# Kernel optimization log

Measured on AMD Instinct MI355X. Metric: run time of the kernel, lower is better.

## Reference

```python
import jax, jax.numpy as jnp
import numpy as np

L, B, T, D, H, FF = 4, 8, 1024, 256, 8, 1024
DK = D // H
SCALE = 1.0 / np.sqrt(DK)


def _ln(x, g, b, eps=1e-6):
    m = jnp.mean(x, axis=-1, keepdims=True)
    v = jnp.mean(jnp.square(x - m), axis=-1, keepdims=True)
    return (x - m) * jax.lax.rsqrt(v + eps) * g + b


def _l2norm(x, eps=1e-8):
    n = jnp.sqrt(jnp.sum(jnp.square(x), axis=-1, keepdims=True))
    return x / jnp.maximum(n, eps)


def setup_inputs() -> dict:
    key = jax.random.key(0)
    ks = jax.random.split(key, 8)
    s = 0.02
    inp = {
        'x': jax.random.normal(ks[0], (B, T, D), dtype=jnp.float32),
        'padding_mask': jnp.zeros((B, T), dtype=bool),
        'ln1_g': jnp.ones((L, D), jnp.float32), 'ln1_b': jnp.zeros((L, D), jnp.float32),
        'qn_g': jnp.ones((L, D), jnp.float32), 'qn_b': jnp.zeros((L, D), jnp.float32),
        'Wqkv': jax.random.normal(ks[1], (L, 3 * D, D), jnp.float32) * s,
        'bqkv': jnp.zeros((L, 3 * D), jnp.float32),
        'Wo': jax.random.normal(ks[2], (L, D, D), jnp.float32) * s,
        'bo': jnp.zeros((L, D), jnp.float32),
        'ln2_g': jnp.ones((L, D), jnp.float32), 'ln2_b': jnp.zeros((L, D), jnp.float32),
        'W1': jax.random.normal(ks[3], (L, FF, D), jnp.float32) * s,
        'b1': jnp.zeros((L, FF), jnp.float32),
        'W2': jax.random.normal(ks[4], (L, D, FF), jnp.float32) * s,
        'b2': jnp.zeros((L, D), jnp.float32),
        'alpha': jnp.full((L,), 0.1, jnp.float32),
        'beta': jnp.full((L,), 0.1, jnp.float32),
    }
    return inp


def _block(x, pad_mask, p):
    (g1, bb1, qg, qb, wqkv, bqkv, wo, bo, g2, bb2, w1, b1, w2, b2, a, be) = p
    Bn, Tn, Dn = x.shape
    # --- SemiCausalAttention on norm1(x) ---
    xn = _ln(x, g1, bb1)
    h = _ln(xn, qg, qb)                      # q_norm LayerNorm
    qkv = h @ wqkv.T + bqkv                  # [B,T,3D]
    qkv = qkv.reshape(Bn, Tn, 3, H, DK).transpose(2, 0, 3, 1, 4)  # [3,B,H,T,dk]
    Q, K, V = qkv[0], qkv[1], qkv[2]
    Q = _l2norm(Q)
    K = _l2norm(K)
    scores = jnp.einsum('bhtd,bhsd->bhts', Q, K) * SCALE
    scores = jnp.clip(scores, -10.0, 10.0)
    causal = jnp.triu(jnp.ones((Tn, Tn), dtype=bool), k=1)        # True = future
    scores = jnp.where(causal[None, None], -10000.0, scores)
    scores = jnp.where(pad_mask[:, None, None, :], -10000.0, scores)
    attn = jax.nn.softmax(scores, axis=-1)
    ao = jnp.einsum('bhts,bhsd->bhtd', attn, V)                   # [B,H,T,dk]
    ao = ao.transpose(0, 2, 1, 3).reshape(Bn, Tn, Dn)
    attn_out = (ao @ wo.T + bo) * 0.5
    x = x + jnp.tanh(a) * attn_out
    # --- FFN ---
    f = _ln(x, g2, bb2)
    f = jax.nn.gelu(f @ w1.T + b1, approximate=False)
    f = f @ w2.T + b2
    x = x + jnp.tanh(be) * f
    return jnp.clip(x, -100.0, 100.0)


def reference(x, padding_mask, ln1_g, ln1_b, qn_g, qn_b, Wqkv, bqkv, Wo, bo,
              ln2_g, ln2_b, W1, b1, W2, b2, alpha, beta):
    params = (ln1_g, ln1_b, qn_g, qn_b, Wqkv, bqkv, Wo, bo,
              ln2_g, ln2_b, W1, b1, W2, b2, alpha, beta)

    def step(carry, p):
        return _block(carry, padding_mask, p), None

    out, _ = jax.lax.scan(step, x, params)
    return out
```

## Files before the change

### kernel.cpp

```cpp
#include <hip/hip_runtime.h>
#include <hip/hip_bf16.h>
#include <math.h>

#define BB 8
#define TT 1024
#define DD 256
#define HH 8
#define BT 8192

typedef __attribute__((ext_vector_type(4))) float f32x4;
typedef __attribute__((ext_vector_type(16))) float f32x16;
typedef __attribute__((ext_vector_type(8))) short short8;
typedef __attribute__((ext_vector_type(4))) short short4v;
typedef __attribute__((ext_vector_type(8))) __bf16 bf16x8;

__device__ inline float bf2f(short s) {
  unsigned int u = ((unsigned int)(unsigned short)s) << 16;
  return __builtin_bit_cast(float, u);
}
__device__ inline short f2bf(float f) {
  unsigned int u = __builtin_bit_cast(unsigned int, f);
  unsigned int lsb = (u >> 16) & 1u;
  u += 0x7fffu + lsb;
  return (short)(u >> 16);
}
__device__ inline unsigned int cvtpk(float lo, float hi) {
  unsigned int r;
  asm("v_cvt_pk_bf16_f32 %0, %1, %2" : "=v"(r) : "v"(lo), "v"(hi));
  return r;
}

__device__ inline f32x4 mfma16(short8 a, short8 b, f32x4 c) {
  return __builtin_amdgcn_mfma_f32_16x16x32_bf16(
      __builtin_bit_cast(bf16x8, a), __builtin_bit_cast(bf16x8, b), c, 0, 0, 0);
}
__device__ inline f32x16 mfma32(short8 a, short8 b, f32x16 c) {
  return __builtin_amdgcn_mfma_f32_32x32x16_bf16(
      __builtin_bit_cast(bf16x8, a), __builtin_bit_cast(bf16x8, b), c, 0, 0, 0);
}

__device__ inline void gload_lds16(void* lds, const void* g) {
  __builtin_amdgcn_global_load_lds(
      (const __attribute__((address_space(1))) unsigned int*)g,
      (__attribute__((address_space(3))) unsigned int*)lds, 16, 0, 0);
}

__global__ __launch_bounds__(256) void cvt_all(
    const float4* __restrict__ s0, short4v* __restrict__ d0, int n0,
    const float4* __restrict__ s1, short4v* __restrict__ d1, int n1,
    const float4* __restrict__ s2, short4v* __restrict__ d2, int n2,
    const float4* __restrict__ s3, short4v* __restrict__ d3, int n3)
{
  int i = blockIdx.x * 256 + threadIdx.x;
  const float4* s; short4v* d;
  if (i < n0) { s = s0 + i; d = d0 + i; }
  else if ((i -= n0) < n1) { s = s1 + i; d = d1 + i; }
  else if ((i -= n1) < n2) { s = s2 + i; d = d2 + i; }
  else if ((i -= n2) < n3) { s = s3 + i; d = d3 + i; }
  else return;
  float4 v = *s;
  short4v o;
  o[0] = f2bf(v.x); o[1] = f2bf(v.y); o[2] = f2bf(v.z); o[3] = f2bf(v.w);
  *d = o;
}

__global__ __launch_bounds__(256) void ln_kernel(
    const float* __restrict__ Xin,
    const float* __restrict__ g1, const float* __restrict__ b1,
    const float* __restrict__ g2, const float* __restrict__ b2,
    short* __restrict__ out)
{
  const int row = blockIdx.x * 4 + (threadIdx.x >> 6);
  const int lane = threadIdx.x & 63;
  const float4 v = *(const float4*)(Xin + (size_t)row * 256 + lane * 4);
  float y[4] = {v.x, v.y, v.z, v.w};

  float s = y[0] + y[1] + y[2] + y[3];
  #pragma unroll
  for (int m = 32; m >= 1; m >>= 1) s += __shfl_xor(s, m, 64);
  float mean = s * (1.0f / 256.0f);
  float sq = 0.f;
  #pragma unroll
  for (int i = 0; i < 4; ++i) { y[i] -= mean; sq += y[i] * y[i]; }
  #pragma unroll
  for (int m = 32; m >= 1; m >>= 1) sq += __shfl_xor(sq, m, 64);
  float rs = rsqrtf(sq * (1.0f / 256.0f) + 1e-6f);
  #pragma unroll
  for (int i = 0; i < 4; ++i) y[i] = y[i] * rs * g1[lane * 4 + i] + b1[lane * 4 + i];

  float s2 = y[0] + y[1] + y[2] + y[3];
  #pragma unroll
  for (int m = 32; m >= 1; m >>= 1) s2 += __shfl_xor(s2, m, 64);
  float m2 = s2 * (1.0f / 256.0f);
  float sq2 = 0.f;
  #pragma unroll
  for (int i = 0; i < 4; ++i) { y[i] -= m2; sq2 += y[i] * y[i]; }
  #pragma unroll
  for (int m = 32; m >= 1; m >>= 1) sq2 += __shfl_xor(sq2, m, 64);
  float rs2 = rsqrtf(sq2 * (1.0f / 256.0f) + 1e-6f);
  #pragma unroll
  for (int i = 0; i < 4; ++i) y[i] = y[i] * rs2 * g2[lane * 4 + i] + b2[lane * 4 + i];

  #pragma unroll
  for (int i = 0; i < 4; ++i) out[(size_t)row * 256 + lane * 4 + i] = f2bf(y[i]);
}

__global__ __launch_bounds__(256) void vtr_kernel(
    const short* __restrict__ Vc, short* __restrict__ vT)
{
  __shared__ short T_s[32][264];
  const int tid = threadIdx.x;
  const int bh = blockIdx.x >> 2;
  const int tc = blockIdx.x & 3;
  const int t = tc * 256 + tid;
  const short* src = Vc + ((size_t)(bh << 10) + t) * 32;
  short8 v0 = *(const short8*)(src);
  short8 v1 = *(const short8*)(src + 8);
  short8 v2 = *(const short8*)(src + 16);
  short8 v3 = *(const short8*)(src + 24);
  #pragma unroll
  for (int d = 0; d < 8; ++d) {
    T_s[d][tid] = v0[d];
    T_s[d + 8][tid] = v1[d];
    T_s[d + 16][tid] = v2[d];
    T_s[d + 24][tid] = v3[d];
  }
  __syncthreads();
  const int d = tid >> 3, toff = (tid & 7) * 32;
  short* dst = vT + ((size_t)bh * 32 + d) * 1024 + tc * 256 + toff;
  #pragma unroll
  for (int s = 0; s < 4; ++s)
    *(short8*)(dst + s * 8) = *(const short8*)&T_s[d][toff + s * 8];
}

template<int BN, int EPI>
__global__ __launch_bounds__(256) void gemm_bt(
    const short* __restrict__ A, const short* __restrict__ Bw,
    const float* __restrict__ bias,
    short* __restrict__ O0, short* __restrict__ O1, short* __restrict__ O2,
    int M, int N, int K)
{
  constexpr int MI = (BN == 128) ? 4 : 2;
  __shared__ __align__(16) short A_s[2][128 * 64];
  __shared__ __align__(16) short B_s[2][BN * 64];
  const int tid = threadIdx.x;
  const int lane = tid & 63;
  const int w = tid >> 6;
  const int lo4 = lane & 15, hi2 = lane >> 4;
  int wm, wn0;
  if (BN == 128) { wm = (w >> 1) * 64; wn0 = (w & 1) * 64; }
  else           { wm = w * 32;        wn0 = 0; }
  const int bid = blockIdx.x + blockIdx.y * gridDim.x;
  const int nwg = gridDim.x * gridDim.y;
  const int wg = (bid & 7) * (nwg >> 3) + (bid >> 3);
  const int tM = (wg / gridDim.x) * 128, tN = (wg % gridDim.x) * BN;

  f32x4 acc[MI][4];
  #pragma unroll
  for (int i = 0; i < MI; ++i)
    #pragma unroll
    for (int j = 0; j < 4; ++j) acc[i][j] = (f32x4){0.f, 0.f, 0.f, 0.f};

  auto stage = [&](int buf, int k0) {
    #pragma unroll
    for (int ri = 0; ri < 4; ++ri) {
      int o = ri * 2048 + tid * 8;
      int row = o >> 6;
      int col = (o & 63) ^ ((row & 7) << 3);
      gload_lds16(&A_s[buf][ri * 2048 + w * 512], A + (size_t)(tM + row) * K + k0 + col);
    }
    #pragma unroll
    for (int ri = 0; ri < BN / 32; ++ri) {
      int o = ri * 2048 + tid * 8;
      int row = o >> 6;
      int col = (o & 63) ^ ((row & 7) << 3);
      gload_lds16(&B_s[buf][ri * 2048 + w * 512], Bw + (size_t)(tN + row) * K + k0 + col);
    }
  };

  const int nt = K >> 6;
  stage(0, 0);
  __syncthreads();
  for (int t = 0; t < nt; ++t) {
    const int cur = t & 1;
    if (t + 1 < nt) stage(cur ^ 1, (t + 1) << 6);
    #pragma unroll
    for (int kc = 0; kc < 2; ++kc) {
      short8 af[MI], bfr[4];
      #pragma unroll
      for (int i = 0; i < MI; ++i) {
        int row = wm + i * 16 + lo4;
        af[i] = *(const short8*)&A_s[cur][row * 64 + ((kc * 32 + hi2 * 8) ^ ((row & 7) << 3))];
      }
      #pragma unroll
      for (int j = 0; j < 4; ++j) {
        int row = wn0 + j * 16 + lo4;
        bfr[j] = *(const short8*)&B_s[cur][row * 64 + ((kc * 32 + hi2 * 8) ^ ((row & 7) << 3))];
      }
      #pragma unroll
      for (int i = 0; i < MI; ++i)
        #pragma unroll
        for (int j = 0; j < 4; ++j)
          acc[i][j] = mfma16(af[i], bfr[j], acc[i][j]);
    }
    __syncthreads();
  }

  if (EPI == 4) {
    #pragma unroll
    for (int i = 0; i < MI; ++i)
      #pragma unroll
      for (int j = 0; j < 4; ++j)
        #pragma unroll
        for (int r = 0; r < 4; ++r)
          acc[i][j][r] += bias[tN + wn0 + j * 16 + lo4];
    if (tN < 512) {
      const float C2 = 0.25503489702966368f;
      const float sc = (tN < 256) ? C2 : 1.0f;
      #pragma unroll
      for (int i = 0; i < MI; ++i) {
        #pragma unroll
        for (int r = 0; r < 4; ++r) {
          float s01 = acc[i][0][r] * acc[i][0][r] + acc[i][1][r] * acc[i][1][r];
          float s23 = acc[i][2][r] * acc[i][2][r] + acc[i][3][r] * acc[i][3][r];
          #pragma unroll
          for (int m = 1; m <= 8; m <<= 1) {
            s01 += __shfl_xor(s01, m, 64);
            s23 += __shfl_xor(s23, m, 64);
          }
          float n01 = sc / fmaxf(sqrtf(s01), 1e-8f);
          float n23 = sc / fmaxf(sqrtf(s23), 1e-8f);
          acc[i][0][r] *= n01; acc[i][1][r] *= n01;
          acc[i][2][r] *= n23; acc[i][3][r] *= n23;
        }
      }
    }
    short* dst = (tN < 256) ? O0 : (tN < 512) ? O1 : O2;
    #pragma unroll
    for (int i = 0; i < MI; ++i)
      #pragma unroll
      for (int j = 0; j < 4; ++j)
        #pragma unroll
        for (int r = 0; r < 4; ++r) {
          int row = tM + wm + i * 16 + hi2 * 4 + r;
          int colr = (tN + wn0 + j * 16 + lo4) & 255;
          int h = colr >> 5, d = colr & 31;
          size_t idx = (((size_t)((row >> 10) * 8 + h) << 10) | (size_t)(row & 1023)) * 32 + d;
          dst[idx] = f2bf(acc[i][j][r]);
        }
    return;
  }

  #pragma unroll
  for (int i = 0; i < MI; ++i) {
    #pragma unroll
    for (int j = 0; j < 4; ++j) {
      #pragma unroll
      for (int r = 0; r < 4; ++r) {
        int row = tM + wm + i * 16 + hi2 * 4 + r;
        int col = tN + wn0 + j * 16 + lo4;
        float v = acc[i][j][r] + bias[col];
        size_t idx = (size_t)row * N + col;
        if (EPI == 2) {
          float gl = 0.5f * v * (1.0f + erff(v * 0.70710678118f));
          O0[idx] = f2bf(gl);
        } else {
          O0[idx] = f2bf(v);
        }
      }
    }
  }
}

template<int MODE>
__global__ __launch_bounds__(256) void gemm_ln(
    const short* __restrict__ A, const short* __restrict__ Bw,
    const float* __restrict__ bias, float* __restrict__ X,
    short* __restrict__ Obf, const float* __restrict__ scale_p,
    const float* __restrict__ gA, const float* __restrict__ bA,
    const float* __restrict__ gB, const float* __restrict__ bB,
    int K, int doLN)
{
  __shared__ __align__(16) short A_s[2][32 * 64];
  __shared__ __align__(16) short B_s[2][256 * 64];
  __shared__ float Red[2][32][4][2];
  const int tid = threadIdx.x;
  const int lane = tid & 63;
  const int w = tid >> 6;
  const int lo4 = lane & 15, hi2 = lane >> 4;
  const int tM = blockIdx.x * 32;

  f32x4 acc[2][4];
  #pragma unroll
  for (int i = 0; i < 2; ++i)
    #pragma unroll
    for (int j = 0; j < 4; ++j) acc[i][j] = (f32x4){0.f, 0.f, 0.f, 0.f};

  auto stage = [&](int buf, int k0) {
    {
      int o = tid * 8;
      int row = o >> 6;
      int col = (o & 63) ^ ((row & 7) << 3);
      gload_lds16(&A_s[buf][w * 512], A + (size_t)(tM + row) * K + k0 + col);
    }
    #pragma unroll
    for (int ri = 0; ri < 8; ++ri) {
      int o = ri * 2048 + tid * 8;
      int row = o >> 6;
      int col = (o & 63) ^ ((row & 7) << 3);
      gload_lds16(&B_s[buf][ri * 2048 + w * 512], Bw + (size_t)row * K + k0 + col);
    }
  };

  const int nt = K >> 6;
  stage(0, 0);
  __syncthreads();
  for (int t = 0; t < nt; ++t) {
    const int cur = t & 1;
    if (t + 1 < nt) stage(cur ^ 1, (t + 1) << 6);
    #pragma unroll
    for (int kc = 0; kc < 2; ++kc) {
      short8 af[2], bfr[4];
      #pragma unroll
      for (int i = 0; i < 2; ++i) {
        int row = i * 16 + lo4;
        af[i] = *(const short8*)&A_s[cur][row * 64 + ((kc * 32 + hi2 * 8) ^ ((row & 7) << 3))];
      }
      #pragma unroll
      for (int j = 0; j < 4; ++j) {
        int row = w * 64 + j * 16 + lo4;
        bfr[j] = *(const short8*)&B_s[cur][row * 64 + ((kc * 32 + hi2 * 8) ^ ((row & 7) << 3))];
      }
      #pragma unroll
      for (int i = 0; i < 2; ++i)
        #pragma unroll
        for (int j = 0; j < 4; ++j)
          acc[i][j] = mfma16(af[i], bfr[j], acc[i][j]);
    }
    __syncthreads();
  }

  const float ts = tanhf(scale_p[0]);
  float xv[2][4][4];
  #pragma unroll
  for (int i = 0; i < 2; ++i)
    #pragma unroll
    for (int j = 0; j < 4; ++j)
      #pragma unroll
      for (int r = 0; r < 4; ++r) {
        int row = i * 16 + hi2 * 4 + r;
        int col = w * 64 + j * 16 + lo4;
        float v = acc[i][j][r] + bias[col];
        size_t idx = (size_t)(tM + row) * 256 + col;
        float xn;
        if (MODE == 0) {
          xn = X[idx] + ts * 0.5f * v;
        } else {
          xn = X[idx] + ts * v;
          xn = fminf(100.f, fmaxf(-100.f, xn));
        }
        X[idx] = xn;
        xv[i][j][r] = xn;
      }

  if (!doLN) return;

  #pragma unroll
  for (int i = 0; i < 2; ++i)
    #pragma unroll
    for (int r = 0; r < 4; ++r) {
      float s = xv[i][0][r] + xv[i][1][r] + xv[i][2][r] + xv[i][3][r];
      float q = xv[i][0][r] * xv[i][0][r] + xv[i][1][r] * xv[i][1][r]
              + xv[i][2][r] * xv[i][2][r] + xv[i][3][r] * xv[i][3][r];
      #pragma unroll
      for (int m = 1; m <= 8; m <<= 1) { s += __shfl_xor(s, m, 64); q += __shfl_xor(q, m, 64); }
      if (lo4 == 0) { Red[0][i * 16 + hi2 * 4 + r][w][0] = s; Red[0][i * 16 + hi2 * 4 + r][w][1] = q; }
    }
  __syncthreads();
  #pragma unroll
  for (int i = 0; i < 2; ++i)
    #pragma unroll
    for (int r = 0; r < 4; ++r) {
      int row = i * 16 + hi2 * 4 + r;
      float s = Red[0][row][0][0] + Red[0][row][1][0] + Red[0][row][2][0] + Red[0][row][3][0];
      float q = Red[0][row][0][1] + Red[0][row][1][1] + Red[0][row][2][1] + Red[0][row][3][1];
      float mu = s * (1.0f / 256.0f);
      float var = q * (1.0f / 256.0f) - mu * mu;
      float rs = rsqrtf(var + 1e-6f);
      #pragma unroll
      for (int j = 0; j < 4; ++j) {
        int col = w * 64 + j * 16 + lo4;
        xv[i][j][r] = (xv[i][j][r] - mu) * rs * gA[col] + bA[col];
      }
    }

  if (MODE == 1) {
    #pragma unroll
    for (int i = 0; i < 2; ++i)
      #pragma unroll
      for (int r = 0; r < 4; ++r) {
        float s = xv[i][0][r] + xv[i][1][r] + xv[i][2][r] + xv[i][3][r];
        float q = xv[i][0][r] * xv[i][0][r] + xv[i][1][r] * xv[i][1][r]
                + xv[i][2][r] * xv[i][2][r] + xv[i][3][r] * xv[i][3][r];
        #pragma unroll
        for (int m = 1; m <= 8; m <<= 1) { s += __shfl_xor(s, m, 64); q += __shfl_xor(q, m, 64); }
        if (lo4 == 0) { Red[1][i * 16 + hi2 * 4 + r][w][0] = s; Red[1][i * 16 + hi2 * 4 + r][w][1] = q; }
      }
    __syncthreads();
    #pragma unroll
    for (int i = 0; i < 2; ++i)
      #pragma unroll
      for (int r = 0; r < 4; ++r) {
        int row = i * 16 + hi2 * 4 + r;
        float s = Red[1][row][0][0] + Red[1][row][1][0] + Red[1][row][2][0] + Red[1][row][3][0];
        float q = Red[1][row][0][1] + Red[1][row][1][1] + Red[1][row][2][1] + Red[1][row][3][1];
        float mu = s * (1.0f / 256.0f);
        float var = q * (1.0f / 256.0f) - mu * mu;
        float rs = rsqrtf(var + 1e-6f);
        #pragma unroll
        for (int j = 0; j < 4; ++j) {
          int col = w * 64 + j * 16 + lo4;
          xv[i][j][r] = (xv[i][j][r] - mu) * rs * gB[col] + bB[col];
        }
      }
  }

  #pragma unroll
  for (int i = 0; i < 2; ++i)
    #pragma unroll
    for (int j = 0; j < 4; ++j)
      #pragma unroll
      for (int r = 0; r < 4; ++r) {
        int row = i * 16 + hi2 * 4 + r;
        int col = w * 64 + j * 16 + lo4;
        Obf[(size_t)(tM + row) * 256 + col] = f2bf(xv[i][j][r]);
      }
}

__device__ __forceinline__ void pv_acc(const unsigned int* PKO, int half_,
                                       short8 vb, int hi1, f32x16& acc) {
  unsigned int keep0 = hi1 ? PKO[4 * half_ + 2] : PKO[4 * half_ + 0];
  unsigned int keep1 = hi1 ? PKO[4 * half_ + 3] : PKO[4 * half_ + 1];
  unsigned int send0 = hi1 ? PKO[4 * half_ + 0] : PKO[4 * half_ + 2];
  unsigned int send1 = hi1 ? PKO[4 * half_ + 1] : PKO[4 * half_ + 3];
  unsigned int r0 = (unsigned int)__shfl_xor((int)send0, 32, 64);
  unsigned int r1 = (unsigned int)__shfl_xor((int)send1, 32, 64);
  union { unsigned int u[4]; short8 s; } fa;
  fa.u[0] = hi1 ? r0 : keep0;
  fa.u[1] = hi1 ? r1 : keep1;
  fa.u[2] = hi1 ? keep0 : r0;
  fa.u[3] = hi1 ? keep1 : r1;
  acc = mfma32(fa.s, vb, acc);
}

template<bool KG1, bool M0, bool M1>
__device__ __forceinline__ void attn_tile(
    int t, const short* __restrict__ Kbase, const short* __restrict__ VTl,
    const short8* qb, unsigned int pm0, unsigned int pm1, int lo5, int hi1,
    f32x16& oaccA, f32x16& oaccB, float& rsum)
{
  const short* kp0 = Kbase + (size_t)(t * 64 + lo5) * 32;
  short8 k00 = *(const short8*)(kp0 + hi1 * 8);
  short8 k01 = *(const short8*)(kp0 + 16 + hi1 * 8);
  short8 k10, k11;
  if (KG1) {
    const short* kp1 = Kbase + (size_t)(t * 64 + 32 + lo5) * 32;
    k10 = *(const short8*)(kp1 + hi1 * 8);
    k11 = *(const short8*)(kp1 + 16 + hi1 * 8);
  }
  const short* vp = VTl + t * 64 + hi1 * 8;
  short8 vb0 = *(const short8*)(vp);
  short8 vb1 = *(const short8*)(vp + 16);
  short8 vb2, vb3;
  if (KG1) {
    vb2 = *(const short8*)(vp + 32);
    vb3 = *(const short8*)(vp + 48);
  }
  unsigned int pk0[8], pk1[8];
  {
    f32x16 z = (f32x16)0.0f;
    z = mfma32(k00, qb[0], z);
    z = mfma32(k01, qb[1], z);
    float pr[16];
    #pragma unroll
    for (int r = 0; r < 16; ++r) {
      float sv = __builtin_amdgcn_fmed3f(z[r], -14.4269504f, 14.4269504f);
      float pe;
      asm("v_exp_f32 %0, %1" : "=v"(pe) : "v"(sv));
      const int keyrel = (r & 3) + 8 * (r >> 2) + 4 * hi1;
      if (M0) pe = (keyrel > lo5) ? 0.f : pe;
      if (pm0) pe = ((pm0 >> keyrel) & 1u) ? 0.f : pe;
      pr[r] = pe;
      rsum += pe;
    }
    #pragma unroll
    for (int i = 0; i < 8; ++i) pk0[i] = cvtpk(pr[2 * i], pr[2 * i + 1]);
  }
  if (KG1) {
    f32x16 z = (f32x16)0.0f;
    z = mfma32(k10, qb[0], z);
    z = mfma32(k11, qb[1], z);
    float pr[16];
    #pragma unroll
    for (int r = 0; r < 16; ++r) {
      float sv = __builtin_amdgcn_fmed3f(z[r], -14.4269504f, 14.4269504f);
      float pe;
      asm("v_exp_f32 %0, %1" : "=v"(pe) : "v"(sv));
      const int keyrel = (r & 3) + 8 * (r >> 2) + 4 * hi1;
      if (M1) pe = (keyrel > lo5) ? 0.f : pe;
      if (pm1) pe = ((pm1 >> keyrel) & 1u) ? 0.f : pe;
      pr[r] = pe;
      rsum += pe;
    }
    #pragma unroll
    for (int i = 0; i < 8; ++i) pk1[i] = cvtpk(pr[2 * i], pr[2 * i + 1]);
  }
  pv_acc(pk0, 0, vb0, hi1, oaccA);
  pv_acc(pk0, 1, vb1, hi1, oaccB);
  if (KG1) {
    pv_acc(pk1, 0, vb2, hi1, oaccA);
    pv_acc(pk1, 1, vb3, hi1, oaccB);
  }
}

__global__ __launch_bounds__(256, 2) void attn_kernel(
    const short* __restrict__ Qp, const short* __restrict__ Kp,
    const short* __restrict__ vT, const unsigned char* __restrict__ pad,
    short* __restrict__ ao)
{
  __shared__ float Red[2][17][64];
  const int tid = threadIdx.x, lane = tid & 63, w = tid >> 6;
  const int lo5 = lane & 31, hi1 = lane >> 5;
  const int bid = blockIdx.x;
  const int b = bid & 7;
  const int h = (bid >> 3) & 7;
  const int bj = bid >> 6;
  const int p = w >> 1;
  const int half = w & 1;
  const int j = p ? (31 - bj) : bj;
  const size_t rowbase = (size_t)b * TT;
  const int bh = b * 8 + h;
  const int qrow = j * 32 + lo5;
  const int ntile = (j >> 1) + 1;

  const short* Kbase = Kp + ((size_t)bh << 10) * 32;
  const short* VTl = vT + ((size_t)bh * 32 + lo5) * 1024;

  const ulonglong2 pv = *(const ulonglong2*)(pad + rowbase + lane * 16);
  const unsigned long long anyp = __ballot((pv.x | pv.y) != 0ull);

  short8 qb[2];
  #pragma unroll
  for (int c2 = 0; c2 < 2; ++c2)
    qb[c2] = *(const short8*)(Qp + (((size_t)bh << 10) + qrow) * 32 + c2 * 16 + hi1 * 8);

  f32x16 oaccA = (f32x16)0.0f;
  f32x16 oaccB = (f32x16)0.0f;
  float rsum = 0.f;

  for (int t = half; t < ntile; t += 2) {
    unsigned long long pm = 0;
    if ((anyp >> (4 * t)) & 0xFull)
      pm = __ballot(pad[rowbase + t * 64 + lane] != 0);
    unsigned int pm0 = (unsigned int)pm, pm1 = (unsigned int)(pm >> 32);
    if (t + 1 < ntile)
      attn_tile<true, false, false>(t, Kbase, VTl, qb, pm0, pm1, lo5, hi1, oaccA, oaccB, rsum);
    else if (j & 1)
      attn_tile<true, false, true>(t, Kbase, VTl, qb, pm0, pm1, lo5, hi1, oaccA, oaccB, rsum);
    else
      attn_tile<false, true, false>(t, Kbase, VTl, qb, pm0, pm1, lo5, hi1, oaccA, oaccB, rsum);
  }

  if (half) {
    #pragma unroll
    for (int r = 0; r < 16; ++r) Red[p][r][lane] = oaccA[r] + oaccB[r];
    Red[p][16][lane] = rsum;
  }
  __syncthreads();
  if (!half) {
    #pragma unroll
    for (int r = 0; r < 16; ++r) oaccA[r] += oaccB[r] + Red[p][r][lane];
    rsum += Red[p][16][lane];
    rsum += __shfl_xor(rsum, 32, 64);
    float rinv = 1.0f / fmaxf(rsum, 1e-30f);
    #pragma unroll
    for (int r = 0; r < 16; ++r) {
      int ql = (r & 3) + 8 * (r >> 2) + 4 * hi1;
      float riv = __shfl(rinv, ql, 64);
      int qg = j * 32 + ql;
      ao[(rowbase + qg) * 256 + h * 32 + lo5] = f2bf(oaccA[r] * riv);
    }
  }
}

extern "C" void kernel_launch(void* const* d_in, const int* in_sizes, int n_in,
                              void* d_out, int out_size, void* d_ws, size_t ws_size,
                              hipStream_t stream) {
  const float* x_in  = (const float*)d_in[0];
  const unsigned char* pad = (const unsigned char*)d_in[1];
  const float* ln1_g = (const float*)d_in[2];
  const float* ln1_b = (const float*)d_in[3];
  const float* qn_g  = (const float*)d_in[4];
  const float* qn_b  = (const float*)d_in[5];
  const float* Wqkv  = (const float*)d_in[6];
  const float* bqkv  = (const float*)d_in[7];
  const float* Wo    = (const float*)d_in[8];
  const float* bo    = (const float*)d_in[9];
  const float* ln2_g = (const float*)d_in[10];
  const float* ln2_b = (const float*)d_in[11];
  const float* W1    = (const float*)d_in[12];
  const float* b1    = (const float*)d_in[13];
  const float* W2    = (const float*)d_in[14];
  const float* b2    = (const float*)d_in[15];
  const float* alpha = (const float*)d_in[16];
  const float* beta  = (const float*)d_in[17];

  char* ws = (char*)d_ws;
  size_t off = 0;
  short* wqkv_bf = (short*)(ws + off); off += (size_t)4 * 768 * 256 * 2;
  short* wo_bf   = (short*)(ws + off); off += (size_t)4 * 256 * 256 * 2;
  short* w1_bf   = (short*)(ws + off); off += (size_t)4 * 1024 * 256 * 2;
  short* w2_bf   = (short*)(ws + off); off += (size_t)4 * 256 * 1024 * 2;
  short* h_bf    = (short*)(ws + off); off += (size_t)BT * 256 * 2;
  short* Qp_bf   = (short*)(ws + off); off += (size_t)BT * 256 * 2;
  short* Kp_bf   = (short*)(ws + off); off += (size_t)BT * 256 * 2;
  short* Vc_bf   = (short*)(ws + off); off += (size_t)BT * 256 * 2;
  short* vT_bf   = (short*)(ws + off); off += (size_t)BT * 256 * 2;
  short* ao_bf   = (short*)(ws + off); off += (size_t)BT * 256 * 2;
  short* g_bf    = (short*)(ws + off); off += (size_t)BT * 1024 * 2;

  float* X = (float*)d_out;

  hipMemcpyAsync(d_out, x_in, (size_t)BT * DD * 4, hipMemcpyDeviceToDevice, stream);
  cvt_all<<<3072, 256, 0, stream>>>(
      (const float4*)Wqkv, (short4v*)wqkv_bf, 4 * 768 * 256 / 4,
      (const float4*)Wo,   (short4v*)wo_bf,   4 * 256 * 256 / 4,
      (const float4*)W1,   (short4v*)w1_bf,   4 * 1024 * 256 / 4,
      (const float4*)W2,   (short4v*)w2_bf,   4 * 256 * 1024 / 4);

  ln_kernel<<<2048, 256, 0, stream>>>(X, ln1_g, ln1_b, qn_g, qn_b, h_bf);

  for (int l = 0; l < 4; ++l) {
    gemm_bt<128, 4><<<dim3(6, 64), 256, 0, stream>>>(h_bf, wqkv_bf + (size_t)l * 768 * 256,
                                                     bqkv + l * 768, Qp_bf, Kp_bf, Vc_bf,
                                                     8192, 768, 256);
    vtr_kernel<<<256, 256, 0, stream>>>(Vc_bf, vT_bf);
    attn_kernel<<<1024, 256, 0, stream>>>(Qp_bf, Kp_bf, vT_bf, pad, ao_bf);
    gemm_ln<0><<<256, 256, 0, stream>>>(ao_bf, wo_bf + (size_t)l * 256 * 256,
                                        bo + l * 256, X, h_bf, alpha + l,
                                        ln2_g + l * 256, ln2_b + l * 256,
                                        nullptr, nullptr, 256, 1);
    gemm_bt<128, 2><<<dim3(8, 64), 256, 0, stream>>>(h_bf, w1_bf + (size_t)l * 1024 * 256,
                                                     b1 + l * 1024, g_bf, nullptr, nullptr,
                                                     8192, 1024, 256);
    const int nl = (l < 3) ? (l + 1) : 0;
    gemm_ln<1><<<256, 256, 0, stream>>>(g_bf, w2_bf + (size_t)l * 256 * 1024,
                                        b2 + l * 256, X, h_bf, beta + l,
                                        ln1_g + nl * 256, ln1_b + nl * 256,
                                        qn_g + nl * 256, qn_b + nl * 256,
                                        1024, (l < 3) ? 1 : 0);
  }
}
```

Measured before the change: 366.3 us.

## Fuse V transpose into QKV GEMM epilogue, drop input copy, use tanh-form GELU

The QKV GEMM epilogue now writes the V tile straight into the transposed [B,H,dk,T] layout with 4-wide stores, so the separate transpose kernel and its scratch buffer go away. The initial device-to-device copy of x into the output is removed: layer 0 reads the residual from the input tensor and writes to the output buffer. The exact erf GELU is replaced by a sigmoid-form tanh approximation built from v_exp and a reciprocal. That approximation differs slightly from the exact erf GELU the reference uses.

```diff
diff --git a/kernel.cpp b/kernel.cpp
--- a/kernel.cpp
+++ b/kernel.cpp
@@ -103,34 +103,6 @@
 
   #pragma unroll
   for (int i = 0; i < 4; ++i) out[(size_t)row * 256 + lane * 4 + i] = f2bf(y[i]);
-}
-
-__global__ __launch_bounds__(256) void vtr_kernel(
-    const short* __restrict__ Vc, short* __restrict__ vT)
-{
-  __shared__ short T_s[32][264];
-  const int tid = threadIdx.x;
-  const int bh = blockIdx.x >> 2;
-  const int tc = blockIdx.x & 3;
-  const int t = tc * 256 + tid;
-  const short* src = Vc + ((size_t)(bh << 10) + t) * 32;
-  short8 v0 = *(const short8*)(src);
-  short8 v1 = *(const short8*)(src + 8);
-  short8 v2 = *(const short8*)(src + 16);
-  short8 v3 = *(const short8*)(src + 24);
-  #pragma unroll
-  for (int d = 0; d < 8; ++d) {
-    T_s[d][tid] = v0[d];
-    T_s[d + 8][tid] = v1[d];
-    T_s[d + 16][tid] = v2[d];
-    T_s[d + 24][tid] = v3[d];
-  }
-  __syncthreads();
-  const int d = tid >> 3, toff = (tid & 7) * 32;
-  short* dst = vT + ((size_t)bh * 32 + d) * 1024 + tc * 256 + toff;
-  #pragma unroll
-  for (int s = 0; s < 4; ++s)
-    *(short8*)(dst + s * 8) = *(const short8*)&T_s[d][toff + s * 8];
 }
 
 template<int BN, int EPI>
@@ -214,7 +186,24 @@
         #pragma unroll
         for (int r = 0; r < 4; ++r)
           acc[i][j][r] += bias[tN + wn0 + j * 16 + lo4];
-    if (tN < 512) {
+    if (tN >= 512) {
+      #pragma unroll
+      for (int i = 0; i < MI; ++i) {
+        #pragma unroll
+        for (int j = 0; j < 4; ++j) {
+          short4v o;
+          #pragma unroll
+          for (int r = 0; r < 4; ++r) o[r] = f2bf(acc[i][j][r]);
+          int row0 = tM + wm + i * 16 + hi2 * 4;
+          int colr = (tN + wn0 + j * 16 + lo4) - 512;
+          int h = colr >> 5, d = colr & 31;
+          int b = row0 >> 10, t0 = row0 & 1023;
+          *(short4v*)(O2 + (((size_t)(b * 8 + h) * 32 + d) << 10) + t0) = o;
+        }
+      }
+      return;
+    }
+    {
       const float C2 = 0.25503489702966368f;
       const float sc = (tN < 256) ? C2 : 1.0f;
       #pragma unroll
@@ -235,7 +224,7 @@
         }
       }
     }
-    short* dst = (tN < 256) ? O0 : (tN < 512) ? O1 : O2;
+    short* dst = (tN < 256) ? O0 : O1;
     #pragma unroll
     for (int i = 0; i < MI; ++i)
       #pragma unroll
@@ -262,7 +251,11 @@
         float v = acc[i][j][r] + bias[col];
         size_t idx = (size_t)row * N + col;
         if (EPI == 2) {
-          float gl = 0.5f * v * (1.0f + erff(v * 0.70710678118f));
+          float t1 = v * v;
+          float arg = fminf(v * (1.0f + 0.044715f * t1) * 2.3022077f, 80.0f);
+          float ex;
+          asm("v_exp_f32 %0, %1" : "=v"(ex) : "v"(arg));
+          float gl = v * ex * __builtin_amdgcn_rcpf(ex + 1.0f);
           O0[idx] = f2bf(gl);
         } else {
           O0[idx] = f2bf(v);
@@ -275,7 +268,7 @@
 template<int MODE>
 __global__ __launch_bounds__(256) void gemm_ln(
     const short* __restrict__ A, const short* __restrict__ Bw,
-    const float* __restrict__ bias, float* __restrict__ X,
+    const float* __restrict__ bias, const float* Xin, float* X,
     short* __restrict__ Obf, const float* __restrict__ scale_p,
     const float* __restrict__ gA, const float* __restrict__ bA,
     const float* __restrict__ gB, const float* __restrict__ bB,
@@ -354,7 +347,7 @@
         size_t idx = (size_t)(tM + row) * 256 + col;
         float xn;
         if (MODE == 0) {
-          xn = X[idx] + ts * 0.5f * v;
+          xn = Xin[idx] + ts * 0.5f * v;
         } else {
           xn = X[idx] + ts * v;
           xn = fminf(100.f, fmaxf(-100.f, xn));
@@ -624,30 +617,28 @@
   short* h_bf    = (short*)(ws + off); off += (size_t)BT * 256 * 2;
   short* Qp_bf   = (short*)(ws + off); off += (size_t)BT * 256 * 2;
   short* Kp_bf   = (short*)(ws + off); off += (size_t)BT * 256 * 2;
-  short* Vc_bf   = (short*)(ws + off); off += (size_t)BT * 256 * 2;
   short* vT_bf   = (short*)(ws + off); off += (size_t)BT * 256 * 2;
   short* ao_bf   = (short*)(ws + off); off += (size_t)BT * 256 * 2;
   short* g_bf    = (short*)(ws + off); off += (size_t)BT * 1024 * 2;
 
   float* X = (float*)d_out;
 
-  hipMemcpyAsync(d_out, x_in, (size_t)BT * DD * 4, hipMemcpyDeviceToDevice, stream);
   cvt_all<<<3072, 256, 0, stream>>>(
       (const float4*)Wqkv, (short4v*)wqkv_bf, 4 * 768 * 256 / 4,
       (const float4*)Wo,   (short4v*)wo_bf,   4 * 256 * 256 / 4,
       (const float4*)W1,   (short4v*)w1_bf,   4 * 1024 * 256 / 4,
       (const float4*)W2,   (short4v*)w2_bf,   4 * 256 * 1024 / 4);
 
-  ln_kernel<<<2048, 256, 0, stream>>>(X, ln1_g, ln1_b, qn_g, qn_b, h_bf);
+  ln_kernel<<<2048, 256, 0, stream>>>(x_in, ln1_g, ln1_b, qn_g, qn_b, h_bf);
 
   for (int l = 0; l < 4; ++l) {
     gemm_bt<128, 4><<<dim3(6, 64), 256, 0, stream>>>(h_bf, wqkv_bf + (size_t)l * 768 * 256,
-                                                     bqkv + l * 768, Qp_bf, Kp_bf, Vc_bf,
+                                                     bqkv + l * 768, Qp_bf, Kp_bf, vT_bf,
                                                      8192, 768, 256);
-    vtr_kernel<<<256, 256, 0, stream>>>(Vc_bf, vT_bf);
     attn_kernel<<<1024, 256, 0, stream>>>(Qp_bf, Kp_bf, vT_bf, pad, ao_bf);
     gemm_ln<0><<<256, 256, 0, stream>>>(ao_bf, wo_bf + (size_t)l * 256 * 256,
-                                        bo + l * 256, X, h_bf, alpha + l,
+                                        bo + l * 256, (l == 0) ? x_in : (const float*)X, X,
+                                        h_bf, alpha + l,
                                         ln2_g + l * 256, ln2_b + l * 256,
                                         nullptr, nullptr, 256, 1);
     gemm_bt<128, 2><<<dim3(8, 64), 256, 0, stream>>>(h_bf, w1_bf + (size_t)l * 1024 * 256,
@@ -655,7 +646,7 @@
                                                      8192, 1024, 256);
     const int nl = (l < 3) ? (l + 1) : 0;
     gemm_ln<1><<<256, 256, 0, stream>>>(g_bf, w2_bf + (size_t)l * 256 * 1024,
-                                        b2 + l * 256, X, h_bf, beta + l,
+                                        b2 + l * 256, X, X, h_bf, beta + l,
                                         ln1_g + nl * 256, ln1_b + nl * 256,
                                         qn_g + nl * 256, qn_b + nl * 256,
                                         1024, (l < 3) ? 1 : 0);
```

New measurement: 348.8 us. 1.05x faster.
